# Optimization experiments

Hardware: AMD Instinct MI355X
Metric: run time of the kernel (lower is better)

## Reference

```python
import jax, jax.numpy as jnp
import numpy as np
from jax import lax


def setup_inputs() -> dict:
    key = jax.random.key(0)
    ks = jax.random.split(key, 16)
    f32 = jnp.float32
    g = lambda k, shp, s=0.02: jax.random.normal(k, shp, dtype=f32) * s
    inp = {
        "x": jax.random.normal(ks[0], (4, 1, 4096), dtype=f32),
        # conv_time: Conv1d(1,128,3,pad=1)
        "conv_time_w": g(ks[1], (128, 1, 3)), "conv_time_b": jnp.zeros((128,), f32),
        "bn0_g": jnp.ones((128,), f32), "bn0_b": jnp.zeros((128,), f32),
        "bn0_m": jnp.zeros((128,), f32), "bn0_v": jnp.ones((128,), f32),
        # block1: Conv1d(128,256,3,pad=1)+BN
        "conv1_w": g(ks[2], (256, 128, 3)), "conv1_b": jnp.zeros((256,), f32),
        "bn1_g": jnp.ones((256,), f32), "bn1_b": jnp.zeros((256,), f32),
        "bn1_m": jnp.zeros((256,), f32), "bn1_v": jnp.ones((256,), f32),
        # block2: Conv1d(256,512,3,pad=1)+BN
        "conv2_w": g(ks[3], (512, 256, 3)), "conv2_b": jnp.zeros((512,), f32),
        "bn2_g": jnp.ones((512,), f32), "bn2_b": jnp.zeros((512,), f32),
        "bn2_m": jnp.zeros((512,), f32), "bn2_v": jnp.ones((512,), f32),
        # GAT 1: fc Linear(512,512), attn_fc Linear(1024,1)
        "gat1_fc_w": g(ks[4], (512, 512)), "gat1_fc_b": jnp.zeros((512,), f32),
        "gat1_attn_w": g(ks[5], (1024,)), "gat1_attn_b": jnp.zeros((), f32),
        # GAT 2: fc Linear(512,256), attn_fc Linear(512,1)
        "gat2_fc_w": g(ks[6], (256, 512)), "gat2_fc_b": jnp.zeros((256,), f32),
        "gat2_attn_w": g(ks[7], (512,)), "gat2_attn_b": jnp.zeros((), f32),
        # head: Linear(256,2)
        "fc_w": g(ks[8], (2, 256)), "fc_b": jnp.zeros((2,), f32),
    }
    return inp


def _conv1d(x, w, b):
    # x: [B,C,T], w: [O,C,3], padding=1
    y = lax.conv_general_dilated(x, w, window_strides=(1,), padding=((1, 1),),
                                 dimension_numbers=("NCH", "OIH", "NCH"))
    return y + b[None, :, None]


def _bn(x, g, b, m, v):
    # eval-mode BatchNorm1d over channel dim
    return (x - m[None, :, None]) * (g * lax.rsqrt(v + 1e-5))[None, :, None] + b[None, :, None]


def _maxpool2(x):
    return lax.reduce_window(x, -jnp.inf, lax.max, (1, 1, 2), (1, 1, 2), "VALID")


def _gat(x2d, fc_w, fc_b, aw, ab):
    # Faithful to: cat([h_i, h_j]) @ attn_w == h_i @ aw[:d] + h_j @ aw[d:]
    h = x2d @ fc_w.T + fc_b           # [N, d]
    d = h.shape[-1]
    s1 = h @ aw[:d]                   # [N] (query part, h.repeat(1,N))
    s2 = h @ aw[d:]                   # [N] (key part,   h.repeat(N,1))
    e = jax.nn.leaky_relu(s1[:, None] + s2[None, :] + ab, negative_slope=0.01)  # [N,N]
    att = jax.nn.softmax(e, axis=1)
    return att @ h                    # [N, d]


def reference(x, conv_time_w, conv_time_b, bn0_g, bn0_b, bn0_m, bn0_v,
              conv1_w, conv1_b, bn1_g, bn1_b, bn1_m, bn1_v,
              conv2_w, conv2_b, bn2_g, bn2_b, bn2_m, bn2_v,
              gat1_fc_w, gat1_fc_b, gat1_attn_w, gat1_attn_b,
              gat2_fc_w, gat2_fc_b, gat2_attn_w, gat2_attn_b,
              fc_w, fc_b):
    h = jax.nn.relu(_bn(_conv1d(x, conv_time_w, conv_time_b), bn0_g, bn0_b, bn0_m, bn0_v))
    h = _maxpool2(jax.nn.relu(_bn(_conv1d(h, conv1_w, conv1_b), bn1_g, bn1_b, bn1_m, bn1_v)))
    h = _maxpool2(jax.nn.relu(_bn(_conv1d(h, conv2_w, conv2_b), bn2_g, bn2_b, bn2_m, bn2_v)))
    h = jnp.transpose(h, (0, 2, 1))   # [B, S, 512]
    B, S, C = h.shape
    g = h.reshape(B * S, C)           # whole batch flattened into one graph (as in source)
    g = _gat(g, gat1_fc_w, gat1_fc_b, gat1_attn_w, gat1_attn_b)   # [N, 512]
    g = _gat(g, gat2_fc_w, gat2_fc_b, gat2_attn_w, gat2_attn_b)   # [N, 256]
    pooled = g.reshape(B, S, -1).mean(axis=1)                     # [B, 256]
    return pooled @ fc_w.T + fc_b     # [B, 2] (dropout is identity in eval)
```

## Files before the change

kernel.cpp:

```cpp
#include <hip/hip_runtime.h>
#include <hip/hip_bf16.h>
#include <math.h>


#define NN 4096
#define BB 4
#define TT0 4096

__global__ void k_conv_time2(const float* __restrict__ x, const float* __restrict__ w,
                             const float* __restrict__ cb, const float* __restrict__ g,
                             const float* __restrict__ bbp, const float* __restrict__ m,
                             const float* __restrict__ v, float* __restrict__ out) {
  int gid = blockIdx.x * 256 + threadIdx.x;
  int t4 = gid & 1023;
  int o = (gid >> 10) & 127;
  int b = gid >> 17;
  int t = t4 * 4;
  float sc = g[o] * rsqrtf(v[o] + 1e-5f);
  float sh = (cb[o] - m[o]) * sc + bbp[o];
  const float* xb = x + b * 4096;
  float4 xc = *(const float4*)&xb[t];
  float xm = (t > 0) ? xb[t - 1] : 0.f;
  float xp = (t + 4 < 4096) ? xb[t + 4] : 0.f;
  const float* wo = w + o * 3;
  float w0 = wo[0], w1 = wo[1], w2 = wo[2];
  float4 y;
  y.x = fmaxf((w0 * xm   + w1 * xc.x + w2 * xc.y) * sc + sh, 0.f);
  y.y = fmaxf((w0 * xc.x + w1 * xc.y + w2 * xc.z) * sc + sh, 0.f);
  y.z = fmaxf((w0 * xc.y + w1 * xc.z + w2 * xc.w) * sc + sh, 0.f);
  y.w = fmaxf((w0 * xc.z + w1 * xc.w + w2 * xp  ) * sc + sh, 0.f);
  *(float4*)&out[((size_t)(b * 128) + o) * 4096 + t] = y;
}

template <int C, int TIN>
__global__ __launch_bounds__(256, 4)
void k_conv_pool9(const float* __restrict__ in, const float* __restrict__ w,
                  const float* __restrict__ cb, const float* __restrict__ g,
                  const float* __restrict__ bbp, const float* __restrict__ m,
                  const float* __restrict__ v, float* __restrict__ out, int OCH) {
  constexpr int TOUT = TIN / 2;
  constexpr int CC = 32;
  __shared__ float xs[CC][264];

  int bx = blockIdx.x;
  int nT = TIN / 256;
  int tb = bx % nT;
  int ob = (bx / nT) % (OCH / 16);
  int b  = bx / (nT * (OCH / 16));
  int tid = threadIdx.x;
  int lane = tid & 63;
  int wv = __builtin_amdgcn_readfirstlane(tid >> 6);
  int t0 = tb * 256;

  float acc[4][4];
  #pragma unroll
  for (int oi = 0; oi < 4; oi++)
    #pragma unroll
    for (int p = 0; p < 4; p++) acc[oi][p] = 0.f;

  const float* wq = w + (size_t)(ob * 16 + wv * 4) * C * 3;

  for (int c0 = 0; c0 < C; c0 += CC) {
    #pragma unroll
    for (int u = 0; u < 9; u++) {
      int e4 = tid + 256 * u;
      if (e4 < CC * 66) {
        int cc = e4 / 66, j4 = e4 - cc * 66;
        int t = t0 - 4 + 4 * j4;
        const float* src = &in[((size_t)(b * C) + cc + c0) * TIN + t];
        float4 val;
        if (t >= 0 && t + 3 < TIN) {
          val = *(const float4*)src;
        } else {
          val.x = (t     >= 0 && t     < TIN) ? src[0] : 0.f;
          val.y = (t + 1 >= 0 && t + 1 < TIN) ? src[1] : 0.f;
          val.z = (t + 2 >= 0 && t + 2 < TIN) ? src[2] : 0.f;
          val.w = (t + 3 >= 0 && t + 3 < TIN) ? src[3] : 0.f;
        }
        *(float4*)&xs[cc][4 * j4] = val;
      }
    }
    __syncthreads();
    #pragma unroll 2
    for (int cc = 0; cc < CC; ++cc) {
      float4 X = *(const float4*)&xs[cc][4 * lane + 4];
      float xbL = xs[cc][3];
      float xbR = xs[cc][260];
      float xm1 = __shfl_up(X.w, 1, 64);
      if (lane == 0) xm1 = xbL;
      float xp4 = __shfl_down(X.x, 1, 64);
      if (lane == 63) xp4 = xbR;
      #pragma unroll
      for (int oi = 0; oi < 4; oi++) {
        const float* wr = wq + ((size_t)oi * C + c0 + cc) * 3;
        float w0 = wr[0], w1 = wr[1], w2 = wr[2];
        acc[oi][0] += w0 * xm1 + w1 * X.x + w2 * X.y;
        acc[oi][1] += w0 * X.x + w1 * X.y + w2 * X.z;
        acc[oi][2] += w0 * X.y + w1 * X.z + w2 * X.w;
        acc[oi][3] += w0 * X.z + w1 * X.w + w2 * xp4;
      }
    }
    __syncthreads();
  }

  int base_o = ob * 16 + wv * 4;
  #pragma unroll
  for (int oi = 0; oi < 4; oi++) {
    int o = base_o + oi;
    float sc = g[o] * rsqrtf(v[o] + 1e-5f);
    float sh = (cb[o] - m[o]) * sc + bbp[o];
    float2 r;
    r.x = fmaxf(fmaxf(acc[oi][0] * sc + sh, acc[oi][1] * sc + sh), 0.f);
    r.y = fmaxf(fmaxf(acc[oi][2] * sc + sh, acc[oi][3] * sc + sh), 0.f);
    *(float2*)&out[((size_t)(b * OCH) + o) * TOUT + tb * 128 + 2 * lane] = r;
  }
}

__global__ __launch_bounds__(512, 1)
void k_gemm_chw(const float* __restrict__ A, const float* __restrict__ Wt,
                const float* __restrict__ bias, float* __restrict__ Cout) {
  constexpr int K = 512, N = 512;
  __shared__ float As[32][132];
  __shared__ float Bs[32][68];
  int i0 = blockIdx.x * 128, j0 = blockIdx.y * 64;
  int tid = threadIdx.x;
  int tx = tid & 15, ty = tid >> 4;
  int b = i0 >> 10, s0 = i0 & 1023;
  const float* Ab = A + (size_t)b * K * 1024 + s0;

  float acc[4][4];
  #pragma unroll
  for (int ii = 0; ii < 4; ii++)
    #pragma unroll
    for (int jj = 0; jj < 4; jj++) acc[ii][jj] = 0.f;

  int ka = (tid + 0) >> 5, i4a = tid & 31;
  int kb = (tid + 512) >> 5, i4b = tid & 31;
  float4 pa0, pa1; float pb[4];

  pa0 = *(const float4*)&Ab[(size_t)ka * 1024 + 4 * i4a];
  pa1 = *(const float4*)&Ab[(size_t)kb * 1024 + 4 * i4b];
  #pragma unroll
  for (int r = 0; r < 4; r++) {
    int e = tid + 512 * r; int j = e >> 5, k = e & 31;
    pb[r] = Wt[(size_t)(j0 + j) * K + k];
  }

  for (int kt = 0; kt < K; kt += 32) {
    *(float4*)&As[ka][4 * i4a] = pa0;
    *(float4*)&As[kb][4 * i4b] = pa1;
    #pragma unroll
    for (int r = 0; r < 4; r++) {
      int e = tid + 512 * r; int j = e >> 5, k = e & 31;
      Bs[k][j] = pb[r];
    }
    __syncthreads();
    int ktn = (kt + 32 < K) ? kt + 32 : 0;
    float4 na0 = *(const float4*)&Ab[(size_t)(ktn + ka) * 1024 + 4 * i4a];
    float4 na1 = *(const float4*)&Ab[(size_t)(ktn + kb) * 1024 + 4 * i4b];
    float nb[4];
    #pragma unroll
    for (int r = 0; r < 4; r++) {
      int e = tid + 512 * r; int j = e >> 5, k = e & 31;
      nb[r] = Wt[(size_t)(j0 + j) * K + ktn + k];
    }
    #pragma unroll 4
    for (int kk = 0; kk < 32; ++kk) {
      float4 a4 = *(const float4*)&As[kk][ty * 4];
      float4 b4 = *(const float4*)&Bs[kk][tx * 4];
      float a[4] = {a4.x, a4.y, a4.z, a4.w};
      float bv[4] = {b4.x, b4.y, b4.z, b4.w};
      #pragma unroll
      for (int ii = 0; ii < 4; ii++)
        #pragma unroll
        for (int jj = 0; jj < 4; jj++) acc[ii][jj] += a[ii] * bv[jj];
    }
    __syncthreads();
    pa0 = na0; pa1 = na1;
    #pragma unroll
    for (int r = 0; r < 4; r++) pb[r] = nb[r];
  }

  float4 bias4 = *(const float4*)&bias[j0 + 4 * tx];
  #pragma unroll
  for (int ii = 0; ii < 4; ii++) {
    int i = i0 + ty * 4 + ii;
    float4 o4;
    o4.x = acc[ii][0] + bias4.x; o4.y = acc[ii][1] + bias4.y;
    o4.z = acc[ii][2] + bias4.z; o4.w = acc[ii][3] + bias4.w;
    *(float4*)&Cout[(size_t)i * N + j0 + 4 * tx] = o4;
  }
}

__global__ __launch_bounds__(256, 2)
void k_gemm_rm(const float* __restrict__ A, const float* __restrict__ Wt,
               const float* __restrict__ bias, float* __restrict__ Cout) {
  constexpr int K = 512, N = 256;
  __shared__ float As[32][68];
  __shared__ float Bs[32][68];
  int i0 = blockIdx.x * 64, j0 = blockIdx.y * 64;
  int tid = threadIdx.x;
  int tx = tid & 15, ty = tid >> 4;

  float acc[4][4];
  #pragma unroll
  for (int ii = 0; ii < 4; ii++)
    #pragma unroll
    for (int jj = 0; jj < 4; jj++) acc[ii][jj] = 0.f;

  float4 pa[2]; float pb[8];
  #pragma unroll
  for (int r = 0; r < 2; r++) {
    int e4 = tid + 256 * r; int i = e4 >> 3, k4 = e4 & 7;
    pa[r] = *(const float4*)&A[(size_t)(i0 + i) * K + 4 * k4];
  }
  #pragma unroll
  for (int r = 0; r < 8; r++) {
    int e = tid + 256 * r; int j = e >> 5, k = e & 31;
    pb[r] = Wt[(size_t)(j0 + j) * K + k];
  }

  for (int kt = 0; kt < K; kt += 32) {
    #pragma unroll
    for (int r = 0; r < 2; r++) {
      int e4 = tid + 256 * r; int i = e4 >> 3, k4 = e4 & 7;
      As[4 * k4 + 0][i] = pa[r].x; As[4 * k4 + 1][i] = pa[r].y;
      As[4 * k4 + 2][i] = pa[r].z; As[4 * k4 + 3][i] = pa[r].w;
    }
    #pragma unroll
    for (int r = 0; r < 8; r++) {
      int e = tid + 256 * r; int j = e >> 5, k = e & 31;
      Bs[k][j] = pb[r];
    }
    __syncthreads();
    int ktn = (kt + 32 < K) ? kt + 32 : 0;
    float4 na[2]; float nb[8];
    #pragma unroll
    for (int r = 0; r < 2; r++) {
      int e4 = tid + 256 * r; int i = e4 >> 3, k4 = e4 & 7;
      na[r] = *(const float4*)&A[(size_t)(i0 + i) * K + ktn + 4 * k4];
    }
    #pragma unroll
    for (int r = 0; r < 8; r++) {
      int e = tid + 256 * r; int j = e >> 5, k = e & 31;
      nb[r] = Wt[(size_t)(j0 + j) * K + ktn + k];
    }
    #pragma unroll 4
    for (int kk = 0; kk < 32; ++kk) {
      float4 a4 = *(const float4*)&As[kk][ty * 4];
      float4 b4 = *(const float4*)&Bs[kk][tx * 4];
      float a[4] = {a4.x, a4.y, a4.z, a4.w};
      float bv[4] = {b4.x, b4.y, b4.z, b4.w};
      #pragma unroll
      for (int ii = 0; ii < 4; ii++)
        #pragma unroll
        for (int jj = 0; jj < 4; jj++) acc[ii][jj] += a[ii] * bv[jj];
    }
    __syncthreads();
    pa[0] = na[0]; pa[1] = na[1];
    #pragma unroll
    for (int r = 0; r < 8; r++) pb[r] = nb[r];
  }

  float4 bias4 = *(const float4*)&bias[j0 + 4 * tx];
  #pragma unroll
  for (int ii = 0; ii < 4; ii++) {
    int i = i0 + ty * 4 + ii;
    float4 o4;
    o4.x = acc[ii][0] + bias4.x; o4.y = acc[ii][1] + bias4.y;
    o4.z = acc[ii][2] + bias4.z; o4.w = acc[ii][3] + bias4.w;
    *(float4*)&Cout[(size_t)i * N + j0 + 4 * tx] = o4;
  }
}

template <int D>
__global__ void k_rowdot(const float* __restrict__ h, const float* __restrict__ aw,
                         float* __restrict__ s1, float* __restrict__ s2,
                         int* __restrict__ rnk) {
  if (blockIdx.x < 16) rnk[blockIdx.x * 256 + threadIdx.x] = 0;
  int wid = threadIdx.x >> 6, lane = threadIdx.x & 63;
  int i = blockIdx.x * 4 + wid;
  const float* hr = h + (size_t)i * D;
  float d1 = 0.f, d2 = 0.f;
  #pragma unroll
  for (int d = lane; d < D; d += 64) {
    float hv = hr[d];
    d1 += hv * aw[d];
    d2 += hv * aw[D + d];
  }
  for (int off = 32; off; off >>= 1) {
    d1 += __shfl_down(d1, off, 64);
    d2 += __shfl_down(d2, off, 64);
  }
  if (lane == 0) { s1[i] = d1; s2[i] = d2; }
}

__global__ void k_rank(const float* __restrict__ s2v, int* __restrict__ rnk) {
  __shared__ float ls[1024];
  int j = blockIdx.x * 256 + threadIdx.x;
  int base = blockIdx.y * 1024;
  float vj = s2v[j];
  for (int e = threadIdx.x; e < 1024; e += 256) ls[e] = s2v[base + e];
  __syncthreads();
  int cnt = 0;
  #pragma unroll 8
  for (int r = 0; r < 1024; ++r) {
    float vr = ls[r];
    cnt += (vr < vj || (vr == vj && (base + r) < j)) ? 1 : 0;
  }
  atomicAdd(&rnk[j], cnt);
}

__global__ void k_scatter(const float* __restrict__ s2v, const int* __restrict__ rnk,
                          float* __restrict__ svals, int* __restrict__ sidx) {
  int j = blockIdx.x * 256 + threadIdx.x;
  int r = rnk[j];
  svals[r] = s2v[j];
  sidx[r] = j;
}

__global__ void k_tw(const float* __restrict__ s1, const float* __restrict__ svals,
                     const float* __restrict__ abp, int* __restrict__ tarr,
                     float* __restrict__ Aarr, float* __restrict__ Barr,
                     float* __restrict__ wp, float* __restrict__ wm) {
  int i = blockIdx.x * 256 + threadIdx.x;
  float ab = abp[0], M2 = svals[NN - 1];
  float alpha = s1[i] + ab;
  float cthr = -alpha;
  int lo = 0, hi = NN;
  while (lo < hi) {
    int mid = (lo + hi) >> 1;
    if (svals[mid] < cthr) lo = mid + 1; else hi = mid;
  }
  tarr[i] = lo;
  float e1 = alpha + M2;
  float gam = fmaxf(e1, 0.01f * e1);
  Aarr[i] = expf(e1 - gam);
  Barr[i] = expf(0.01f * e1 - gam);
  float d = svals[i] - M2;
  wp[i] = expf(d);
  wm[i] = expf(0.01f * d);
}

__global__ void k_scan_den(const float* __restrict__ wp, const float* __restrict__ wm,
                           float* __restrict__ preden, float* __restrict__ sufden) {
  __shared__ float csP[256], csM[256];
  int tid = threadIdx.x;
  int base = tid * 16;
  float sm = 0.f, sp = 0.f;
  for (int u = 0; u < 16; u++) { sm += wm[base + u]; sp += wp[base + u]; }
  csM[tid] = sm; csP[tid] = sp;
  __syncthreads();
  float offM = 0.f;
  for (int c = 0; c < tid; c++) offM += csM[c];
  float offP = 0.f;
  for (int c = tid + 1; c < 256; c++) offP += csP[c];
  float run = offM;
  for (int u = 0; u < 16; u++) { preden[base + u] = run; run += wm[base + u]; }
  if (tid == 255) preden[NN] = run;
  float runp = offP;
  if (tid == 255) sufden[NN] = 0.f;
  for (int u = 15; u >= 0; u--) { runp += wp[base + u]; sufden[base + u] = runp; }
}

template <int D>
__global__ void k_chunksum(const float* __restrict__ h, const int* __restrict__ sidx,
                           const float* __restrict__ wp, const float* __restrict__ wm,
                           float* __restrict__ csP, float* __restrict__ csM) {
  constexpr int CPT = D / 256;
  int c = blockIdx.x, tid = threadIdx.x;
  __shared__ int lidx[32];
  __shared__ float lwp[32], lwm[32];
  if (tid < 32) {
    int r = c * 32 + tid;
    lidx[tid] = sidx[r]; lwp[tid] = wp[r]; lwm[tid] = wm[r];
  }
  __syncthreads();
  float aP[CPT], aM[CPT];
  #pragma unroll
  for (int q = 0; q < CPT; q++) { aP[q] = 0.f; aM[q] = 0.f; }
  for (int u = 0; u < 32; u++) {
    const float* hr = h + (size_t)lidx[u] * D;
    float fp = lwp[u], fm = lwm[u];
    #pragma unroll
    for (int q = 0; q < CPT; q++) {
      float hv = hr[tid + q * 256];
      aP[q] += fp * hv; aM[q] += fm * hv;
    }
  }
  #pragma unroll
  for (int q = 0; q < CPT; q++) {
    csP[(size_t)c * D + tid + q * 256] = aP[q];
    csM[(size_t)c * D + tid + q * 256] = aM[q];
  }
}

template <int D>
__global__ void k_chunkoff(const float* __restrict__ csP, const float* __restrict__ csM,
                           float* __restrict__ offP, float* __restrict__ offM) {
  int d = blockIdx.x * 256 + threadIdx.x;
  float rm = 0.f;
  for (int cb = 0; cb < 128; cb += 16) {
    float vals[16];
    #pragma unroll
    for (int u = 0; u < 16; u++) vals[u] = csM[(size_t)(cb + u) * D + d];
    #pragma unroll
    for (int u = 0; u < 16; u++) { offM[(size_t)(cb + u) * D + d] = rm; rm += vals[u]; }
  }
  float rp = 0.f;
  for (int cb = 127; cb >= 15; cb -= 16) {
    float vals[16];
    #pragma unroll
    for (int u = 0; u < 16; u++) vals[u] = csP[(size_t)(cb - u) * D + d];
    #pragma unroll
    for (int u = 0; u < 16; u++) { offP[(size_t)(cb - u) * D + d] = rp; rp += vals[u]; }
  }
}

template <int D>
__global__ void k_scanwrite(const float* __restrict__ h, const int* __restrict__ sidx,
                            const float* __restrict__ wp, const float* __restrict__ wm,
                            const float* __restrict__ offP, const float* __restrict__ offM,
                            float* __restrict__ Pre, float* __restrict__ Suf) {
  constexpr int CPT = D / 256;
  int c = blockIdx.x, tid = threadIdx.x;
  __shared__ int lidx[32];
  __shared__ float lwp[32], lwm[32];
  if (tid < 32) {
    int r = c * 32 + tid;
    lidx[tid] = sidx[r]; lwp[tid] = wp[r]; lwm[tid] = wm[r];
  }
  __syncthreads();
  float runM[CPT], runP[CPT];
  #pragma unroll
  for (int q = 0; q < CPT; q++) {
    int d = tid + q * 256;
    runM[q] = offM[(size_t)c * D + d];
    runP[q] = offP[(size_t)c * D + d];
  }
  for (int u = 0; u < 32; u++) {
    const float* hr = h + (size_t)lidx[u] * D;
    float fm = lwm[u];
    #pragma unroll
    for (int q = 0; q < CPT; q++) {
      int d = tid + q * 256;
      Pre[(size_t)(c * 32 + u) * D + d] = runM[q];
      runM[q] += fm * hr[d];
    }
  }
  if (c == 127) {
    #pragma unroll
    for (int q = 0; q < CPT; q++) Pre[(size_t)NN * D + tid + q * 256] = runM[q];
    #pragma unroll
    for (int q = 0; q < CPT; q++) Suf[(size_t)NN * D + tid + q * 256] = 0.f;
  }
  for (int u = 31; u >= 0; u--) {
    const float* hr = h + (size_t)lidx[u] * D;
    float fp = lwp[u];
    #pragma unroll
    for (int q = 0; q < CPT; q++) {
      int d = tid + q * 256;
      runP[q] += fp * hr[d];
      Suf[(size_t)(c * 32 + u) * D + d] = runP[q];
    }
  }
}

template <int D>
__global__ void k_apply(const float* __restrict__ Pre, const float* __restrict__ Suf,
                        const float* __restrict__ preden, const float* __restrict__ sufden,
                        const int* __restrict__ tarr, const float* __restrict__ Aarr,
                        const float* __restrict__ Barr, float* __restrict__ outg) {
  int i = blockIdx.x;
  int t = tarr[i];
  float A = Aarr[i], Bv = Barr[i];
  float den = A * sufden[t] + Bv * preden[t];
  float inv = 1.f / den;
  const float* Pr = Pre + (size_t)t * D;
  const float* Sr = Suf + (size_t)t * D;
  for (int d = threadIdx.x; d < D; d += 256)
    outg[(size_t)i * D + d] = (A * Sr[d] + Bv * Pr[d]) * inv;
}

__global__ void k_pool(const float* __restrict__ g2, float* __restrict__ pp) {
  int b = blockIdx.x >> 4, ch = blockIdx.x & 15;
  const float* base = g2 + ((size_t)(b * 1024) + ch * 64) * 256 + threadIdx.x;
  float s = 0.f;
  for (int r = 0; r < 64; r++) s += base[(size_t)r * 256];
  pp[(size_t)blockIdx.x * 256 + threadIdx.x] = s;
}

__global__ void k_head2(const float* __restrict__ pp, const float* __restrict__ fcw,
                        const float* __restrict__ fcb, float* __restrict__ out) {
  __shared__ float pooled[4][256];
  int tid = threadIdx.x;
  for (int b = 0; b < 4; b++) {
    float s = 0.f;
    for (int ch = 0; ch < 16; ch++) s += pp[(size_t)(b * 16 + ch) * 256 + tid];
    pooled[b][tid] = s * (1.f / 1024.f);
  }
  __syncthreads();
  if (tid < 8) {
    int b = tid >> 1, c = tid & 1;
    float acc = fcb[c];
    for (int cc = 0; cc < 256; cc++) acc += pooled[b][cc] * fcw[c * 256 + cc];
    out[b * 2 + c] = acc;
  }
}

extern "C" void kernel_launch(void* const* d_in, const int* in_sizes, int n_in,
                              void* d_out, int out_size, void* d_ws, size_t ws_size,
                              hipStream_t stream) {
  const float* x    = (const float*)d_in[0];
  const float* ctw  = (const float*)d_in[1];
  const float* ctb  = (const float*)d_in[2];
  const float* bn0g = (const float*)d_in[3];
  const float* bn0b = (const float*)d_in[4];
  const float* bn0m = (const float*)d_in[5];
  const float* bn0v = (const float*)d_in[6];
  const float* c1w  = (const float*)d_in[7];
  const float* c1b  = (const float*)d_in[8];
  const float* bn1g = (const float*)d_in[9];
  const float* bn1b = (const float*)d_in[10];
  const float* bn1m = (const float*)d_in[11];
  const float* bn1v = (const float*)d_in[12];
  const float* c2w  = (const float*)d_in[13];
  const float* c2b  = (const float*)d_in[14];
  const float* bn2g = (const float*)d_in[15];
  const float* bn2b = (const float*)d_in[16];
  const float* bn2m = (const float*)d_in[17];
  const float* bn2v = (const float*)d_in[18];
  const float* g1w  = (const float*)d_in[19];
  const float* g1b  = (const float*)d_in[20];
  const float* g1aw = (const float*)d_in[21];
  const float* g1ab = (const float*)d_in[22];
  const float* g2w  = (const float*)d_in[23];
  const float* g2b  = (const float*)d_in[24];
  const float* g2aw = (const float*)d_in[25];
  const float* g2ab = (const float*)d_in[26];
  const float* fcw  = (const float*)d_in[27];
  const float* fcb  = (const float*)d_in[28];
  float* ws = (float*)d_ws;

  const size_t SLOT = (size_t)(NN + 1) * 512;
  float* slot0 = ws;
  float* slot1 = ws + SLOT;
  float* slot2 = ws + 2 * SLOT;
  float* slot3 = ws + 3 * SLOT;
  float* sm    = ws + 4 * SLOT;
  float* s1    = sm;
  float* s2    = sm + 4096;
  float* svals = sm + 8192;
  int*   sidx  = (int*)(sm + 12288);
  int*   tarr  = (int*)(sm + 16384);
  float* Aarr  = sm + 20480;
  float* Barr  = sm + 24576;
  float* wp    = sm + 28672;
  float* wm    = sm + 32768;
  float* preden = sm + 36864;
  float* sufden = sm + 40968;
  float* csP   = sm + 45072;
  float* csM   = csP + 65536;
  float* offP  = csM + 65536;
  float* offM  = offP + 65536;
  int*   rnk   = (int*)(offM + 65536);
  float* pp    = offM + 65536 + 4096;

  k_conv_time2<<<BB * 128 * 1024 / 256, 256, 0, stream>>>(x, ctw, ctb, bn0g, bn0b, bn0m, bn0v, slot0);
  k_conv_pool9<128, 4096><<<BB * 16 * 16, 256, 0, stream>>>(
      slot0, c1w, c1b, bn1g, bn1b, bn1m, bn1v, slot1, 256);
  k_conv_pool9<256, 2048><<<BB * 32 * 8, 256, 0, stream>>>(
      slot1, c2w, c2b, bn2g, bn2b, bn2m, bn2v, slot2, 512);

  k_gemm_chw<<<dim3(32, 8), 512, 0, stream>>>(slot2, g1w, g1b, slot3);
  k_rowdot<512><<<NN / 4, 256, 0, stream>>>(slot3, g1aw, s1, s2, rnk);
  k_rank<<<dim3(16, 4), 256, 0, stream>>>(s2, rnk);
  k_scatter<<<16, 256, 0, stream>>>(s2, rnk, svals, sidx);
  k_tw<<<NN / 256, 256, 0, stream>>>(s1, svals, g1ab, tarr, Aarr, Barr, wp, wm);
  k_scan_den<<<1, 256, 0, stream>>>(wp, wm, preden, sufden);
  k_chunksum<512><<<128, 256, 0, stream>>>(slot3, sidx, wp, wm, csP, csM);
  k_chunkoff<512><<<2, 256, 0, stream>>>(csP, csM, offP, offM);
  k_scanwrite<512><<<128, 256, 0, stream>>>(slot3, sidx, wp, wm, offP, offM, slot1, slot0);
  k_apply<512><<<NN, 256, 0, stream>>>(slot1, slot0, preden, sufden, tarr, Aarr, Barr, slot2);

  k_gemm_rm<<<dim3(64, 4), 256, 0, stream>>>(slot2, g2w, g2b, slot3);
  k_rowdot<256><<<NN / 4, 256, 0, stream>>>(slot3, g2aw, s1, s2, rnk);
  k_rank<<<dim3(16, 4), 256, 0, stream>>>(s2, rnk);
  k_scatter<<<16, 256, 0, stream>>>(s2, rnk, svals, sidx);
  k_tw<<<NN / 256, 256, 0, stream>>>(s1, svals, g2ab, tarr, Aarr, Barr, wp, wm);
  k_scan_den<<<1, 256, 0, stream>>>(wp, wm, preden, sufden);
  k_chunksum<256><<<128, 256, 0, stream>>>(slot3, sidx, wp, wm, csP, csM);
  k_chunkoff<256><<<1, 256, 0, stream>>>(csP, csM, offP, offM);
  k_scanwrite<256><<<128, 256, 0, stream>>>(slot3, sidx, wp, wm, offP, offM, slot1, slot0);
  k_apply<256><<<NN, 256, 0, stream>>>(slot1, slot0, preden, sufden, tarr, Aarr, Barr, slot2);

  k_pool<<<BB * 16, 256, 0, stream>>>(slot2, pp);
  k_head2<<<1, 256, 0, stream>>>(pp, fcw, fcb, (float*)d_out);
}
```

Before: 413.3 us.

## Pad activation rows and replace LDS-tiled conv with direct-load single-wave conv

The time conv now writes zero-padded rows (stride 4104), and the first fused conv also writes padded output rows, so the next conv can read halos with unconditional vector loads. The LDS-staged, four-wave conv+pool kernel becomes a single-wave kernel that reads each input row straight from global memory with one-step prefetch and computes 8 output channels per thread, removing shared-memory staging and block barriers. Launch bounds on the two GEMMs are also raised to allow more resident blocks. The trade is heavier reliance on cache hits for the input rows, since each wave re-reads them from global memory, plus more register pressure from the 8x4 accumulators.

```diff
diff --git a/kernel.cpp b/kernel.cpp
--- a/kernel.cpp
+++ b/kernel.cpp
@@ -5,9 +5,8 @@
 
 #define NN 4096
 #define BB 4
-#define TT0 4096
-
-__global__ void k_conv_time2(const float* __restrict__ x, const float* __restrict__ w,
+
+__global__ void k_conv_time3(const float* __restrict__ x, const float* __restrict__ w,
                              const float* __restrict__ cb, const float* __restrict__ g,
                              const float* __restrict__ bbp, const float* __restrict__ m,
                              const float* __restrict__ v, float* __restrict__ out) {
@@ -29,94 +28,84 @@
   y.y = fmaxf((w0 * xc.x + w1 * xc.y + w2 * xc.z) * sc + sh, 0.f);
   y.z = fmaxf((w0 * xc.y + w1 * xc.z + w2 * xc.w) * sc + sh, 0.f);
   y.w = fmaxf((w0 * xc.z + w1 * xc.w + w2 * xp  ) * sc + sh, 0.f);
-  *(float4*)&out[((size_t)(b * 128) + o) * 4096 + t] = y;
-}
-
-template <int C, int TIN>
-__global__ __launch_bounds__(256, 4)
-void k_conv_pool9(const float* __restrict__ in, const float* __restrict__ w,
+  float* orow = out + ((size_t)(b * 128) + o) * 4104 + 4;
+  *(float4*)&orow[t] = y;
+  if (t4 == 0)    { orow[-4] = 0.f; orow[-3] = 0.f; orow[-2] = 0.f; orow[-1] = 0.f; }
+  if (t4 == 1023) { orow[4096] = 0.f; orow[4097] = 0.f; orow[4098] = 0.f; orow[4099] = 0.f; }
+}
+
+template <int C, int TIN, int OPAD>
+__global__ __launch_bounds__(64, 2)
+void k_conv_fused(const float* __restrict__ in, const float* __restrict__ w,
                   const float* __restrict__ cb, const float* __restrict__ g,
                   const float* __restrict__ bbp, const float* __restrict__ m,
                   const float* __restrict__ v, float* __restrict__ out, int OCH) {
   constexpr int TOUT = TIN / 2;
-  constexpr int CC = 32;
-  __shared__ float xs[CC][264];
-
+  constexpr int IST = TIN + 8;
+  const int OST = TOUT + 2 * OPAD;
+  int nT = TIN / 256;
   int bx = blockIdx.x;
-  int nT = TIN / 256;
   int tb = bx % nT;
-  int ob = (bx / nT) % (OCH / 16);
-  int b  = bx / (nT * (OCH / 16));
-  int tid = threadIdx.x;
-  int lane = tid & 63;
-  int wv = __builtin_amdgcn_readfirstlane(tid >> 6);
+  int oq = (bx / nT) % (OCH / 8);
+  int b  = bx / (nT * (OCH / 8));
+  int lane = threadIdx.x;
   int t0 = tb * 256;
 
-  float acc[4][4];
-  #pragma unroll
-  for (int oi = 0; oi < 4; oi++)
+  float acc[8][4];
+  #pragma unroll
+  for (int oi = 0; oi < 8; oi++)
     #pragma unroll
     for (int p = 0; p < 4; p++) acc[oi][p] = 0.f;
 
-  const float* wq = w + (size_t)(ob * 16 + wv * 4) * C * 3;
-
-  for (int c0 = 0; c0 < C; c0 += CC) {
-    #pragma unroll
-    for (int u = 0; u < 9; u++) {
-      int e4 = tid + 256 * u;
-      if (e4 < CC * 66) {
-        int cc = e4 / 66, j4 = e4 - cc * 66;
-        int t = t0 - 4 + 4 * j4;
-        const float* src = &in[((size_t)(b * C) + cc + c0) * TIN + t];
-        float4 val;
-        if (t >= 0 && t + 3 < TIN) {
-          val = *(const float4*)src;
-        } else {
-          val.x = (t     >= 0 && t     < TIN) ? src[0] : 0.f;
-          val.y = (t + 1 >= 0 && t + 1 < TIN) ? src[1] : 0.f;
-          val.z = (t + 2 >= 0 && t + 2 < TIN) ? src[2] : 0.f;
-          val.w = (t + 3 >= 0 && t + 3 < TIN) ? src[3] : 0.f;
-        }
-        *(float4*)&xs[cc][4 * j4] = val;
-      }
-    }
-    __syncthreads();
-    #pragma unroll 2
-    for (int cc = 0; cc < CC; ++cc) {
-      float4 X = *(const float4*)&xs[cc][4 * lane + 4];
-      float xbL = xs[cc][3];
-      float xbR = xs[cc][260];
-      float xm1 = __shfl_up(X.w, 1, 64);
-      if (lane == 0) xm1 = xbL;
-      float xp4 = __shfl_down(X.x, 1, 64);
-      if (lane == 63) xp4 = xbR;
-      #pragma unroll
-      for (int oi = 0; oi < 4; oi++) {
-        const float* wr = wq + ((size_t)oi * C + c0 + cc) * 3;
-        float w0 = wr[0], w1 = wr[1], w2 = wr[2];
-        acc[oi][0] += w0 * xm1 + w1 * X.x + w2 * X.y;
-        acc[oi][1] += w0 * X.x + w1 * X.y + w2 * X.z;
-        acc[oi][2] += w0 * X.y + w1 * X.z + w2 * X.w;
-        acc[oi][3] += w0 * X.z + w1 * X.w + w2 * xp4;
-      }
-    }
-    __syncthreads();
-  }
-
-  int base_o = ob * 16 + wv * 4;
-  #pragma unroll
-  for (int oi = 0; oi < 4; oi++) {
+  const float* wq = w + (size_t)(oq * 8) * C * 3;
+  const float* xb = in + (size_t)(b * C) * IST + 4 + t0 + 4 * lane;
+
+  float4 A = *(const float4*)(xb - 1);
+  float2 Bv = *(const float2*)(xb + 3);
+  for (int cc = 0; cc < C; ++cc) {
+    float4 An; float2 Bn;
+    if (cc + 1 < C) {
+      const float* nx = xb + (size_t)(cc + 1) * IST;
+      An = *(const float4*)(nx - 1);
+      Bn = *(const float2*)(nx + 3);
+    }
+    const float* wr = wq + (size_t)cc * 3;
+    #pragma unroll
+    for (int oi = 0; oi < 8; oi++) {
+      const float* wo = wr + (size_t)oi * C * 3;
+      float w0 = wo[0], w1 = wo[1], w2 = wo[2];
+      acc[oi][0] += w0 * A.x + w1 * A.y + w2 * A.z;
+      acc[oi][1] += w0 * A.y + w1 * A.z + w2 * A.w;
+      acc[oi][2] += w0 * A.z + w1 * A.w + w2 * Bv.x;
+      acc[oi][3] += w0 * A.w + w1 * Bv.x + w2 * Bv.y;
+    }
+    A = An; Bv = Bn;
+  }
+
+  int base_o = oq * 8;
+  #pragma unroll
+  for (int oi = 0; oi < 8; oi++) {
     int o = base_o + oi;
     float sc = g[o] * rsqrtf(v[o] + 1e-5f);
     float sh = (cb[o] - m[o]) * sc + bbp[o];
     float2 r;
     r.x = fmaxf(fmaxf(acc[oi][0] * sc + sh, acc[oi][1] * sc + sh), 0.f);
     r.y = fmaxf(fmaxf(acc[oi][2] * sc + sh, acc[oi][3] * sc + sh), 0.f);
-    *(float2*)&out[((size_t)(b * OCH) + o) * TOUT + tb * 128 + 2 * lane] = r;
-  }
-}
-
-__global__ __launch_bounds__(512, 1)
+    *(float2*)&out[((size_t)(b * OCH) + o) * OST + OPAD + tb * 128 + 2 * lane] = r;
+  }
+  if (OPAD > 0 && tb == 0) {
+    if (lane < 8) {
+      float* row = out + ((size_t)(b * OCH) + base_o + lane) * OST;
+      row[0] = 0.f; row[1] = 0.f; row[2] = 0.f; row[3] = 0.f;
+    } else if (lane < 16) {
+      float* row = out + ((size_t)(b * OCH) + base_o + lane - 8) * OST;
+      row[OPAD + TOUT + 0] = 0.f; row[OPAD + TOUT + 1] = 0.f;
+      row[OPAD + TOUT + 2] = 0.f; row[OPAD + TOUT + 3] = 0.f;
+    }
+  }
+}
+
+__global__ __launch_bounds__(512, 4)
 void k_gemm_chw(const float* __restrict__ A, const float* __restrict__ Wt,
                 const float* __restrict__ bias, float* __restrict__ Cout) {
   constexpr int K = 512, N = 512;
@@ -192,7 +181,7 @@
   }
 }
 
-__global__ __launch_bounds__(256, 2)
+__global__ __launch_bounds__(256, 4)
 void k_gemm_rm(const float* __restrict__ A, const float* __restrict__ Wt,
                const float* __restrict__ bias, float* __restrict__ Cout) {
   constexpr int K = 512, N = 256;
@@ -542,12 +531,14 @@
   const float* fcb  = (const float*)d_in[28];
   float* ws = (float*)d_ws;
 
+  const size_t S0SZ = (size_t)4 * 128 * 4104;
+  const size_t S1SZ = (size_t)4 * 256 * 2056;
   const size_t SLOT = (size_t)(NN + 1) * 512;
   float* slot0 = ws;
-  float* slot1 = ws + SLOT;
-  float* slot2 = ws + 2 * SLOT;
-  float* slot3 = ws + 3 * SLOT;
-  float* sm    = ws + 4 * SLOT;
+  float* slot1 = ws + S0SZ;
+  float* slot2 = slot1 + S1SZ;
+  float* slot3 = slot2 + SLOT;
+  float* sm    = slot3 + SLOT;
   float* s1    = sm;
   float* s2    = sm + 4096;
   float* svals = sm + 8192;
@@ -566,10 +557,10 @@
   int*   rnk   = (int*)(offM + 65536);
   float* pp    = offM + 65536 + 4096;
 
-  k_conv_time2<<<BB * 128 * 1024 / 256, 256, 0, stream>>>(x, ctw, ctb, bn0g, bn0b, bn0m, bn0v, slot0);
-  k_conv_pool9<128, 4096><<<BB * 16 * 16, 256, 0, stream>>>(
+  k_conv_time3<<<BB * 128 * 1024 / 256, 256, 0, stream>>>(x, ctw, ctb, bn0g, bn0b, bn0m, bn0v, slot0);
+  k_conv_fused<128, 4096, 4><<<BB * 32 * 16, 64, 0, stream>>>(
       slot0, c1w, c1b, bn1g, bn1b, bn1m, bn1v, slot1, 256);
-  k_conv_pool9<256, 2048><<<BB * 32 * 8, 256, 0, stream>>>(
+  k_conv_fused<256, 2048, 0><<<BB * 64 * 8, 64, 0, stream>>>(
       slot1, c2w, c2b, bn2g, bn2b, bn2m, bn2v, slot2, 512);
 
   k_gemm_chw<<<dim3(32, 8), 512, 0, stream>>>(slot2, g1w, g1b, slot3);
```

Result: faster. 397.4 us (-3.8%).
